# Kernel optimization log

Measured on AMD Instinct MI355X. Metric: run time of the kernel, lower is better.

The kernel has to match this reference:

```python
import jax, jax.numpy as jnp
import numpy as np

EPS = 1e-8
ALPHA = 0.3
PATTERN_W = 0.1


def setup_inputs() -> dict:
    key = jax.random.key(0)
    ks = jax.random.split(key, 6)
    H, W, D, Hid = 1024, 1024, 32, 64
    return {
        "grid_states": jax.random.normal(ks[0], (H, W, D), dtype=jnp.float32),
        "potentials": jax.random.uniform(ks[1], (H, W), dtype=jnp.float32),
        "W1": jax.random.normal(ks[2], (D + 1, Hid), dtype=jnp.float32) * 0.1,
        "b1": jax.random.normal(ks[3], (Hid,), dtype=jnp.float32) * 0.1,
        "W2": jax.random.normal(ks[4], (Hid, D), dtype=jnp.float32) * 0.1,
        "b2": jax.random.normal(ks[5], (D,), dtype=jnp.float32) * 0.1,
    }


def reference(grid_states, potentials, W1, b1, W2, b2):
    # self_similarity: A^3 normalized to unit length, rescaled by ||A||
    cube = grid_states * grid_states * grid_states                     # [H,W,D]
    cube_norm = jnp.linalg.norm(cube, axis=-1, keepdims=True)          # [H,W,1]
    cell_norm = jnp.linalg.norm(grid_states, axis=-1, keepdims=True)   # [H,W,1]
    self_pattern = cube / (cube_norm + EPS) * cell_norm                # [H,W,D]

    cell_with_pattern = grid_states + PATTERN_W * self_pattern         # [H,W,D]

    # transform_net on [cell_with_pattern ; potential]
    x = jnp.concatenate([cell_with_pattern, potentials[..., None]], axis=-1)  # [H,W,D+1]
    h = jax.nn.relu(jnp.einsum("hwc,cf->hwf", x, W1) + b1)             # [H,W,Hid]
    transformed = jnp.einsum("hwf,fd->hwd", h, W2) + b2                # [H,W,D]

    # new_state = transform + alpha * cell  (neighbor influence path only
    # affects role_value, which forward() discards)
    return transformed + ALPHA * grid_states
```

## Files before the change

kernel.cpp:

```cpp
#include <hip/hip_runtime.h>

#define DIM   32
#define HID   64
#define TILES 8

typedef __attribute__((ext_vector_type(8))) short bf16x8;
typedef __attribute__((ext_vector_type(4))) float f32x4;

__device__ __forceinline__ unsigned cvt_pk_bf16(float lo, float hi) {
    unsigned r;
    asm("v_cvt_pk_bf16_f32 %0, %1, %2" : "=v"(r) : "v"(lo), "v"(hi));
    return r;
}
__device__ __forceinline__ float bfp_lo(unsigned u) { return __uint_as_float(u << 16); }
__device__ __forceinline__ float bfp_hi(unsigned u) { return __uint_as_float(u & 0xFFFF0000u); }

__device__ __forceinline__ void plswap(unsigned &a, unsigned &b) {
    auto r = __builtin_amdgcn_permlane32_swap((int)a, (int)b, false, false);
    a = (unsigned)r[0];
    b = (unsigned)r[1];
}

struct f2 { float a, b; };
__device__ __forceinline__ f2 plswap16v(float a, float b) {
    auto r = __builtin_amdgcn_permlane16_swap(__float_as_int(a), __float_as_int(b),
                                              false, false);
    return { __int_as_float(r[0]), __int_as_float(r[1]) };
}

__device__ __forceinline__ float quad_sum(float x) {
    auto r1 = __builtin_amdgcn_permlane32_swap(__float_as_int(x), __float_as_int(x),
                                               false, false);
    float t = __int_as_float(r1[0]) + __int_as_float(r1[1]);
    auto r2 = __builtin_amdgcn_permlane16_swap(__float_as_int(t), __float_as_int(t),
                                               false, false);
    return __int_as_float(r2[0]) + __int_as_float(r2[1]);
}

union bfu { bf16x8 v; unsigned u[4]; };

__global__ __launch_bounds__(128, 3) void behavior_mfma(
    const float* __restrict__ g_in,
    const float* __restrict__ pot,
    const float* __restrict__ W1,
    const float* __restrict__ b1,
    const float* __restrict__ W2,
    const float* __restrict__ b2,
    float* __restrict__ out)
{
    const int tid  = threadIdx.x;
    const int lane = tid & 63;
    const int quad = lane >> 4;
    const int mrow = lane & 15;
    const int wave = tid >> 6;

    const long cell0 = ((long)blockIdx.x * 2 + wave) * (TILES * 16);

    float4 gA[3], gB[3]; float pV[3];
    auto loadT = [&](int s, long cb) {
        const float* gp = g_in + (cb + mrow) * DIM + quad * 8;
        gA[s] = ((const float4*)gp)[0];
        gB[s] = ((const float4*)gp)[1];
        pV[s] = pot[cb + mrow];
    };
    loadT(0, cell0);
    loadT(1, cell0 + 16);
    loadT(2, cell0 + 32);

    bf16x8 w1f[4];
    #pragma unroll
    for (int nb = 0; nb < 4; ++nb) {
        bfu t;
        #pragma unroll
        for (int jp = 0; jp < 4; ++jp)
            t.u[jp] = cvt_pk_bf16(W1[(quad * 8 + 2 * jp)     * HID + nb * 16 + mrow],
                                  W1[(quad * 8 + 2 * jp + 1) * HID + nb * 16 + mrow]);
        w1f[nb] = t.v;
    }
    bf16x8 w2f[2][2];
    #pragma unroll
    for (int kc = 0; kc < 2; ++kc)
        #pragma unroll
        for (int nc = 0; nc < 2; ++nc) {
            bfu t;
            #pragma unroll
            for (int jp = 0; jp < 4; ++jp) {
                const int j0 = 2 * jp;
                const int r0 = kc * 32 + (quad >> 1) * 16 + (quad & 1) * 4
                             + ((j0 >> 2) << 3) + (j0 & 3);
                t.u[jp] = cvt_pk_bf16(W2[r0 * DIM + nc * 16 + mrow],
                                      W2[(r0 + 1) * DIM + nc * 16 + mrow]);
            }
            w2f[kc][nc] = t.v;
        }
    bf16x8 aid[2];
    #pragma unroll
    for (int nc = 0; nc < 2; ++nc) {
        bfu t;
        #pragma unroll
        for (int jp = 0; jp < 4; ++jp) {
            unsigned lo = (quad * 8 + 2 * jp     == nc * 16 + mrow) ? 0x00003F80u : 0u;
            unsigned hi = (quad * 8 + 2 * jp + 1 == nc * 16 + mrow) ? 0x3F800000u : 0u;
            t.u[jp] = lo | hi;
        }
        aid[nc] = t.v;
    }
    unsigned w1pp[4][2], b1p[4][2];
    #pragma unroll
    for (int nb = 0; nb < 4; ++nb)
        #pragma unroll
        for (int p = 0; p < 2; ++p) {
            w1pp[nb][p] = cvt_pk_bf16(W1[32 * HID + nb * 16 + quad * 4 + 2 * p],
                                      W1[32 * HID + nb * 16 + quad * 4 + 2 * p + 1]);
            b1p[nb][p]  = cvt_pk_bf16(b1[nb * 16 + quad * 4 + 2 * p],
                                      b1[nb * 16 + quad * 4 + 2 * p + 1]);
        }
    unsigned b2p[2][2];
    #pragma unroll
    for (int nc = 0; nc < 2; ++nc)
        #pragma unroll
        for (int p = 0; p < 2; ++p)
            b2p[nc][p] = cvt_pk_bf16(b2[nc * 16 + quad * 4 + 2 * p],
                                     b2[nc * 16 + quad * 4 + 2 * p + 1]);

    auto stageA = [&](int s, bfu& h0, bfu& h1, bfu& gf) {
        const float4 a = gA[s], b = gB[s];
        const float potv = pV[s];

        float gv[8] = {a.x, a.y, a.z, a.w, b.x, b.y, b.z, b.w};
        float cube[8];
        float tp = 0.f, sp = 0.f;
        #pragma unroll
        for (int j = 0; j < 8; ++j) {
            float gc = gv[j];
            float g2 = gc * gc;
            float g3 = g2 * gc;
            tp += g2;
            sp = fmaf(g3, g3, sp);
            cube[j] = g3;
        }
        tp = quad_sum(tp);
        sp = quad_sum(sp);
        const float scale = 0.1f * __builtin_amdgcn_sqrtf(tp) *
                            __builtin_amdgcn_rcpf(__builtin_amdgcn_sqrtf(sp) + 1e-8f);

        bfu xf;
        #pragma unroll
        for (int jp = 0; jp < 4; ++jp) {
            xf.u[jp] = cvt_pk_bf16(fmaf(scale, cube[2 * jp],     gv[2 * jp]),
                                   fmaf(scale, cube[2 * jp + 1], gv[2 * jp + 1]));
            gf.u[jp] = cvt_pk_bf16(0.3f * gv[2 * jp], 0.3f * gv[2 * jp + 1]);
        }

        unsigned P[4][2];
        #pragma unroll
        for (int nb = 0; nb < 4; ++nb) {
            f32x4 c1;
            c1[0] = fmaf(potv, bfp_lo(w1pp[nb][0]), bfp_lo(b1p[nb][0]));
            c1[1] = fmaf(potv, bfp_hi(w1pp[nb][0]), bfp_hi(b1p[nb][0]));
            c1[2] = fmaf(potv, bfp_lo(w1pp[nb][1]), bfp_lo(b1p[nb][1]));
            c1[3] = fmaf(potv, bfp_hi(w1pp[nb][1]), bfp_hi(b1p[nb][1]));
            c1 = __builtin_amdgcn_mfma_f32_16x16x32_bf16(w1f[nb], xf.v, c1, 0, 0, 0);
            P[nb][0] = cvt_pk_bf16(fmaxf(c1[0], 0.f), fmaxf(c1[1], 0.f));
            P[nb][1] = cvt_pk_bf16(fmaxf(c1[2], 0.f), fmaxf(c1[3], 0.f));
        }

        {
            unsigned x0 = P[0][0], y0 = P[1][0]; plswap(x0, y0);
            unsigned x1 = P[0][1], y1 = P[1][1]; plswap(x1, y1);
            h0.u[0] = x0; h0.u[1] = x1; h0.u[2] = y0; h0.u[3] = y1;
        }
        {
            unsigned x0 = P[2][0], y0 = P[3][0]; plswap(x0, y0);
            unsigned x1 = P[2][1], y1 = P[3][1]; plswap(x1, y1);
            h1.u[0] = x0; h1.u[1] = x1; h1.u[2] = y0; h1.u[3] = y1;
        }
    };

    auto gemm2st = [&](const bfu& h0, const bfu& h1, const bfu& gf, long cb) {
        f32x4 A, B;
        #pragma unroll
        for (int nc = 0; nc < 2; ++nc) {
            f32x4 c2;
            c2[0] = bfp_lo(b2p[nc][0]);
            c2[1] = bfp_hi(b2p[nc][0]);
            c2[2] = bfp_lo(b2p[nc][1]);
            c2[3] = bfp_hi(b2p[nc][1]);
            c2 = __builtin_amdgcn_mfma_f32_16x16x32_bf16(aid[nc],    gf.v, c2, 0, 0, 0);
            c2 = __builtin_amdgcn_mfma_f32_16x16x32_bf16(w2f[0][nc], h0.v, c2, 0, 0, 0);
            c2 = __builtin_amdgcn_mfma_f32_16x16x32_bf16(w2f[1][nc], h1.v, c2, 0, 0, 0);
            if (nc == 0) A = c2; else B = c2;
        }
        #pragma unroll
        for (int r = 0; r < 4; ++r) {
            float ar = A[r], br = B[r];
            f2 sw = plswap16v(ar, br);
            A[r] = sw.a; B[r] = sw.b;
        }
        const int colq = ((quad & 1) << 4) | ((quad >> 1) << 3);
        float* op = out + (cb + mrow) * DIM + colq;
        *(f32x4*)op       = A;
        *(f32x4*)(op + 4) = B;
    };

    bfu h0P, h1P, gfP;
    stageA(0, h0P, h1P, gfP);
    loadT(0, cell0 + (long)3 * 16);

    #pragma unroll
    for (int t = 1; t < TILES; ++t) {
        const int s = t % 3;
        bfu h0C, h1C, gfC;
        stageA(s, h0C, h1C, gfC);
        if (t + 3 < TILES) loadT(s, cell0 + (long)(t + 3) * 16);
        gemm2st(h0P, h1P, gfP, cell0 + (long)(t - 1) * 16);
        h0P = h0C; h1P = h1C; gfP = gfC;
    }
    gemm2st(h0P, h1P, gfP, cell0 + (long)(TILES - 1) * 16);
}

extern "C" void kernel_launch(void* const* d_in, const int* in_sizes, int n_in,
                              void* d_out, int out_size, void* d_ws, size_t ws_size,
                              hipStream_t stream) {
    const float* g_in = (const float*)d_in[0];
    const float* pot  = (const float*)d_in[1];
    const float* W1   = (const float*)d_in[2];
    const float* b1   = (const float*)d_in[3];
    const float* W2   = (const float*)d_in[4];
    const float* b2   = (const float*)d_in[5];
    float* out = (float*)d_out;

    const int n_cells = in_sizes[1];
    const int cells_per_block = 2 * TILES * 16;
    const int blocks = (n_cells + cells_per_block - 1) / cells_per_block;

    behavior_mfma<<<blocks, 128, 0, stream>>>(g_in, pot, W1, b1, W2, b2, out);
}
```

Before: 247.8 us.

## Switch to single-wave blocks with paired-tile double-buffered pipeline

Blocks shrink from two waves to one, and each wave now covers 128 cells instead of 128 per wave. The old three-stage software pipeline, which overlapped stageA of one tile with the second GEMM of the previous tile, is replaced. The new loop double-buffers loads for pairs of 16-cell tiles and runs two independent stageA/gemm2 chains per iteration to expose ILP. This doubles the grid size and drops the cross-tile overlap, but raises the number of independent MFMA chains per iteration and loosens register pressure from the old pipelining.

```diff
diff --git a/kernel.cpp b/kernel.cpp
--- a/kernel.cpp
+++ b/kernel.cpp
@@ -2,7 +2,6 @@
 
 #define DIM   32
 #define HID   64
-#define TILES 8
 
 typedef __attribute__((ext_vector_type(8))) short bf16x8;
 typedef __attribute__((ext_vector_type(4))) float f32x4;
@@ -39,7 +38,7 @@
 
 union bfu { bf16x8 v; unsigned u[4]; };
 
-__global__ __launch_bounds__(128, 3) void behavior_mfma(
+__global__ __launch_bounds__(64, 3) void behavior_mfma(
     const float* __restrict__ g_in,
     const float* __restrict__ pot,
     const float* __restrict__ W1,
@@ -48,24 +47,24 @@
     const float* __restrict__ b2,
     float* __restrict__ out)
 {
-    const int tid  = threadIdx.x;
-    const int lane = tid & 63;
+    const int lane = threadIdx.x & 63;
     const int quad = lane >> 4;
     const int mrow = lane & 15;
-    const int wave = tid >> 6;
-
-    const long cell0 = ((long)blockIdx.x * 2 + wave) * (TILES * 16);
-
-    float4 gA[3], gB[3]; float pV[3];
-    auto loadT = [&](int s, long cb) {
-        const float* gp = g_in + (cb + mrow) * DIM + quad * 8;
-        gA[s] = ((const float4*)gp)[0];
-        gB[s] = ((const float4*)gp)[1];
-        pV[s] = pot[cb + mrow];
+
+    const long cell0 = (long)blockIdx.x * 128;
+
+    float4 gA[2][2], gB[2][2]; float pV[2][2];
+    auto loadPair = [&](int s, long cb) {
+        #pragma unroll
+        for (int u = 0; u < 2; ++u) {
+            const float* gp = g_in + (cb + u * 16 + mrow) * DIM + quad * 8;
+            gA[s][u] = ((const float4*)gp)[0];
+            gB[s][u] = ((const float4*)gp)[1];
+            pV[s][u] = pot[cb + u * 16 + mrow];
+        }
     };
-    loadT(0, cell0);
-    loadT(1, cell0 + 16);
-    loadT(2, cell0 + 32);
+    loadPair(0, cell0);
+    loadPair(1, cell0 + 32);
 
     bf16x8 w1f[4];
     #pragma unroll
@@ -123,10 +122,7 @@
             b2p[nc][p] = cvt_pk_bf16(b2[nc * 16 + quad * 4 + 2 * p],
                                      b2[nc * 16 + quad * 4 + 2 * p + 1]);
 
-    auto stageA = [&](int s, bfu& h0, bfu& h1, bfu& gf) {
-        const float4 a = gA[s], b = gB[s];
-        const float potv = pV[s];
-
+    auto stageA = [&](float4 a, float4 b, float potv, bfu& h0, bfu& h1, bfu& gf) {
         float gv[8] = {a.x, a.y, a.z, a.w, b.x, b.y, b.z, b.w};
         float cube[8];
         float tp = 0.f, sp = 0.f;
@@ -203,20 +199,21 @@
         *(f32x4*)(op + 4) = B;
     };
 
-    bfu h0P, h1P, gfP;
-    stageA(0, h0P, h1P, gfP);
-    loadT(0, cell0 + (long)3 * 16);
-
-    #pragma unroll
-    for (int t = 1; t < TILES; ++t) {
-        const int s = t % 3;
-        bfu h0C, h1C, gfC;
-        stageA(s, h0C, h1C, gfC);
-        if (t + 3 < TILES) loadT(s, cell0 + (long)(t + 3) * 16);
-        gemm2st(h0P, h1P, gfP, cell0 + (long)(t - 1) * 16);
-        h0P = h0C; h1P = h1C; gfP = gfC;
+    #pragma unroll
+    for (int it = 0; it < 4; ++it) {
+        const int s = it & 1;
+        const float4 a0 = gA[s][0], b0 = gB[s][0]; const float p0 = pV[s][0];
+        const float4 a1 = gA[s][1], b1x = gB[s][1]; const float p1 = pV[s][1];
+        if (it + 2 < 4) loadPair(s, cell0 + (long)(it + 2) * 32);
+
+        bfu h00, h01, g0, h10, h11, g1;
+        stageA(a0, b0,  p0, h00, h01, g0);
+        stageA(a1, b1x, p1, h10, h11, g1);
+
+        const long cb = cell0 + (long)it * 32;
+        gemm2st(h00, h01, g0, cb);
+        gemm2st(h10, h11, g1, cb + 16);
     }
-    gemm2st(h0P, h1P, gfP, cell0 + (long)(TILES - 1) * 16);
 }
 
 extern "C" void kernel_launch(void* const* d_in, const int* in_sizes, int n_in,
@@ -231,8 +228,8 @@
     float* out = (float*)d_out;
 
     const int n_cells = in_sizes[1];
-    const int cells_per_block = 2 * TILES * 16;
+    const int cells_per_block = 128;
     const int blocks = (n_cells + cells_per_block - 1) / cells_per_block;
 
-    behavior_mfma<<<blocks, 128, 0, stream>>>(g_in, pot, W1, b1, W2, b2, out);
-}
+    behavior_mfma<<<blocks, 64, 0, stream>>>(g_in, pot, W1, b1, W2, b2, out);
+}
```

Result: no change. 245.8 us (-0.8%).
